# Optimization experiments

Measured on AMD Instinct MI355X. Metric: run time of the kernel, lower is better.

## Reference

```python
import jax, jax.numpy as jnp
import numpy as np

B, S, D_IN, D_OUT, HID, E, SHARE, TOPK = 4, 2048, 1024, 1024, 2048, 8, 1, 2


def setup_inputs() -> dict:
    key = jax.random.key(0)
    ks = jax.random.split(key, 12)
    s_in = 1.0 / np.sqrt(D_IN)
    s_hid = 1.0 / np.sqrt(HID)
    return {
        "x": jax.random.normal(ks[0], (B, S, D_IN), jnp.float32),
        "gate_w": jax.random.normal(ks[1], (D_IN, E), jnp.float32) * s_in,
        "gate_b": jnp.zeros((E,), jnp.float32),
        "ew1": jax.random.normal(ks[2], (E, D_IN, HID), jnp.float32) * s_in,
        "eb1": jnp.zeros((E, HID), jnp.float32),
        "ew2": jax.random.normal(ks[3], (E, HID, D_OUT), jnp.float32) * s_hid,
        "eb2": jnp.zeros((E, D_OUT), jnp.float32),
        "sw1": jax.random.normal(ks[4], (SHARE, D_IN, HID), jnp.float32) * s_in,
        "sb1": jnp.zeros((SHARE, HID), jnp.float32),
        "sw2": jax.random.normal(ks[5], (SHARE, HID, D_OUT), jnp.float32) * s_hid,
        "sb2": jnp.zeros((SHARE, D_OUT), jnp.float32),
        "top_k": TOPK,
    }


def reference(x, gate_w, gate_b, ew1, eb1, ew2, eb2, sw1, sb1, sw2, sb2, top_k):
    Bx, Sx, Din = x.shape
    flat_x = x.reshape(-1, Din)                      # [T, D]
    T = flat_x.shape[0]
    Ex = gate_w.shape[1]

    # gate + softmax + top-k, renormalize top-k weights
    logits = flat_x @ gate_w + gate_b                # [T, E]
    expert_weights = jax.nn.softmax(logits, axis=-1)
    topv, topi = jax.lax.top_k(expert_weights, top_k)
    topv = topv / jnp.sum(topv, axis=-1, keepdims=True)

    # per-token combine weights scattered into [T, E] (zero for unselected)
    combine = jnp.zeros((T, Ex), flat_x.dtype)
    combine = combine.at[jnp.arange(T)[:, None], topi].add(topv)

    # expert MLPs (BasicExpert: Linear -> ReLU -> Linear), batched over experts
    h = jax.nn.relu(jnp.einsum("td,edh->teh", flat_x, ew1) + eb1)   # [T, E, H]
    eo = jnp.einsum("teh,eho->teo", h, ew2) + eb2                    # [T, E, O]
    moe_out = jnp.einsum("teo,te->to", eo, combine)                  # [T, O]
    final = moe_out.reshape(Bx, Sx, -1)

    # shared experts added densely to every token
    for k in range(sw1.shape[0]):
        sh = jax.nn.relu(jnp.einsum("bsd,dh->bsh", x, sw1[k]) + sb1[k])
        final = final + jnp.einsum("bsh,ho->bso", sh, sw2[k]) + sb2[k]

    return final, expert_weights
```

## Files before the change

### kernel.cpp

```cpp
#include <hip/hip_runtime.h>
#include <hip/hip_bf16.h>
#include <stdint.h>

#define T_TOK 8192
#define DIN   1024
#define DOUT  1024
#define HID   2048
#define NEXP  8
#define MAXN  8192

typedef __attribute__((ext_vector_type(8))) short short8;
typedef __attribute__((ext_vector_type(4))) float floatx4;

__device__ __forceinline__ ushort f2bf(float f) {
    uint32_t u = __float_as_uint(f);
    uint32_t r = (u + 0x7fffu + ((u >> 16) & 1u)) >> 16;
    return (ushort)r;
}

__global__ void convert_x_kernel(const float* __restrict__ in, ushort* __restrict__ out, int n4) {
    int i = blockIdx.x * blockDim.x + threadIdx.x;
    if (i >= n4) return;
    float4 v = ((const float4*)in)[i];
    ushort4 o;
    o.x = f2bf(v.x); o.y = f2bf(v.y); o.z = f2bf(v.z); o.w = f2bf(v.w);
    ((ushort4*)out)[i] = o;
}

__global__ void transpose_bf16_kernel(const float* __restrict__ in, ushort* __restrict__ out,
                                      int R, int C) {
    __shared__ float tile[64][65];
    size_t base = (size_t)blockIdx.z * R * C;
    in  += base;
    out += base;
    int r0 = blockIdx.y * 64, c0 = blockIdx.x * 64;
    int t  = threadIdx.x;
    int rr = t >> 4;
    int cc = (t & 15) * 4;
    for (int p = 0; p < 4; p++) {
        int row = rr + p * 16;
        float4 v = *(const float4*)(in + (size_t)(r0 + row) * C + c0 + cc);
        tile[row][cc + 0] = v.x; tile[row][cc + 1] = v.y;
        tile[row][cc + 2] = v.z; tile[row][cc + 3] = v.w;
    }
    __syncthreads();
    for (int p = 0; p < 4; p++) {
        int orow = rr + p * 16;
        ushort4 o;
        o.x = f2bf(tile[cc + 0][orow]);
        o.y = f2bf(tile[cc + 1][orow]);
        o.z = f2bf(tile[cc + 2][orow]);
        o.w = f2bf(tile[cc + 3][orow]);
        *(ushort4*)(out + (size_t)(c0 + orow) * R + r0 + cc) = o;
    }
}

__global__ void gate_kernel(const float* __restrict__ x, const float* __restrict__ gw,
                            const float* __restrict__ gb, float* __restrict__ ew_out,
                            int* __restrict__ counts, int* __restrict__ expert_tok,
                            float* __restrict__ expert_w) {
    int gid  = blockIdx.x * blockDim.x + threadIdx.x;
    int t    = gid >> 6;
    int lane = threadIdx.x & 63;
    if (t >= T_TOK) return;
    float acc[8];
    #pragma unroll
    for (int e = 0; e < 8; e++) acc[e] = 0.f;
    const float* xrow = x + (size_t)t * DIN;
    #pragma unroll
    for (int i = 0; i < 16; i++) {
        int d = lane + i * 64;
        float xv = xrow[d];
        const float4* wr = (const float4*)(gw + (size_t)d * 8);
        float4 w0 = wr[0], w1 = wr[1];
        acc[0] += xv * w0.x; acc[1] += xv * w0.y; acc[2] += xv * w0.z; acc[3] += xv * w0.w;
        acc[4] += xv * w1.x; acc[5] += xv * w1.y; acc[6] += xv * w1.z; acc[7] += xv * w1.w;
    }
    #pragma unroll
    for (int e = 0; e < 8; e++)
        #pragma unroll
        for (int off = 32; off; off >>= 1) acc[e] += __shfl_xor(acc[e], off);
    if (lane == 0) {
        float l[8], mx = -1e30f;
        #pragma unroll
        for (int e = 0; e < 8; e++) { l[e] = acc[e] + gb[e]; mx = fmaxf(mx, l[e]); }
        float s = 0.f;
        #pragma unroll
        for (int e = 0; e < 8; e++) { l[e] = expf(l[e] - mx); s += l[e]; }
        float inv = 1.f / s;
        #pragma unroll
        for (int e = 0; e < 8; e++) { l[e] *= inv; ew_out[(size_t)t * 8 + e] = l[e]; }
        int i1 = 0;
        #pragma unroll
        for (int e = 1; e < 8; e++) if (l[e] > l[i1]) i1 = e;
        int i2 = (i1 == 0) ? 1 : 0;
        #pragma unroll
        for (int e = 0; e < 8; e++) if (e != i1 && l[e] > l[i2]) i2 = e;
        float s2 = l[i1] + l[i2];
        float w1v = l[i1] / s2, w2v = l[i2] / s2;
        int r1 = atomicAdd(&counts[i1], 1);
        expert_tok[i1 * MAXN + r1] = t;
        expert_w [i1 * MAXN + r1] = w1v;
        int r2 = atomicAdd(&counts[i2], 1);
        expert_tok[i2 * MAXN + r2] = t;
        expert_w [i2 * MAXN + r2] = w2v;
    }
}

__global__ void prefix_kernel(const int* __restrict__ counts, int* __restrict__ offsets) {
    if (threadIdx.x == 0 && blockIdx.x == 0) {
        int o = 0;
        for (int e = 0; e < NEXP; e++) { offsets[e] = o; o += counts[e]; }
    }
}

template <int MODE>
__global__ __launch_bounds__(256)
void gemm_kernel(const ushort* __restrict__ A, const ushort* __restrict__ Bt,
                 const float* __restrict__ bias, ushort* __restrict__ Hout,
                 float* __restrict__ Out,
                 const int* __restrict__ counts, const int* __restrict__ offsets,
                 const int* __restrict__ expert_tok, const float* __restrict__ expert_w,
                 int K) {
    const int e = blockIdx.z;
    int cnt, rowbase = 0;
    size_t bt_off = 0;
    const float* bcol = bias;
    if constexpr (MODE == 0) {
        cnt = counts[e]; rowbase = offsets[e];
        bt_off = (size_t)e * HID * DIN; bcol = bias + (size_t)e * HID;
    } else if constexpr (MODE == 1) {
        cnt = T_TOK;
    } else if constexpr (MODE == 2) {
        cnt = counts[e]; rowbase = offsets[e];
        bt_off = (size_t)e * DOUT * HID; bcol = bias + (size_t)e * DOUT;
    } else {
        cnt = T_TOK;
    }

    const int m0 = blockIdx.y * 128;
    if (m0 >= cnt) return;
    const int n0 = blockIdx.x * 128;

    __shared__ ushort As[128][72];
    __shared__ ushort Bs[128][72];
    __shared__ int    rowA[128];
    __shared__ int    rowTok[128];
    __shared__ float  rowW[128];

    const int tid = threadIdx.x;
    if (tid < 128) {
        int g = m0 + tid;
        if constexpr (MODE == 0) {
            rowA[tid] = (g < cnt) ? expert_tok[e * MAXN + g] : 0;
        } else if constexpr (MODE == 1) {
            rowA[tid] = g;
        } else if constexpr (MODE == 2) {
            rowA[tid]   = (g < cnt) ? (rowbase + g) : rowbase;
            rowTok[tid] = (g < cnt) ? expert_tok[e * MAXN + g] : 0;
            rowW[tid]   = (g < cnt) ? expert_w[e * MAXN + g] : 0.f;
        } else {
            rowA[tid] = g;
        }
    }
    __syncthreads();

    floatx4 acc[4][4];
    #pragma unroll
    for (int i = 0; i < 4; i++)
        #pragma unroll
        for (int j = 0; j < 4; j++) acc[i][j] = (floatx4){0.f, 0.f, 0.f, 0.f};

    const int wave = tid >> 6, lane = tid & 63;
    const int wm = (wave >> 1) * 64, wn = (wave & 1) * 64;
    const int lm = lane & 15, lq = lane >> 4;
    const int arow_s = tid >> 3;
    const int achunk = (tid & 7) * 8;

    for (int k0 = 0; k0 < K; k0 += 64) {
        #pragma unroll
        for (int i = 0; i < 4; i++) {
            int r = arow_s + i * 32;
            const ushort* srca = A + (size_t)rowA[r] * K + k0 + achunk;
            *(uint4*)(&As[r][achunk]) = *(const uint4*)srca;
            const ushort* srcb = Bt + bt_off + (size_t)(n0 + r) * K + k0 + achunk;
            *(uint4*)(&Bs[r][achunk]) = *(const uint4*)srcb;
        }
        __syncthreads();
        #pragma unroll
        for (int kk = 0; kk < 64; kk += 32) {
            short8 afr[4], bfr[4];
            #pragma unroll
            for (int mt = 0; mt < 4; mt++)
                afr[mt] = *(const short8*)(&As[wm + mt * 16 + lm][kk + lq * 8]);
            #pragma unroll
            for (int nt = 0; nt < 4; nt++)
                bfr[nt] = *(const short8*)(&Bs[wn + nt * 16 + lm][kk + lq * 8]);
            #pragma unroll
            for (int mt = 0; mt < 4; mt++)
                #pragma unroll
                for (int nt = 0; nt < 4; nt++)
                    acc[mt][nt] = __builtin_amdgcn_mfma_f32_16x16x32_bf16(
                        afr[mt], bfr[nt], acc[mt][nt], 0, 0, 0);
        }
        __syncthreads();
    }

    #pragma unroll
    for (int mt = 0; mt < 4; mt++) {
        int rl_base = wm + mt * 16 + lq * 4;
        #pragma unroll
        for (int nt = 0; nt < 4; nt++) {
            int col = n0 + wn + nt * 16 + lm;
            float bv = bcol[col];
            #pragma unroll
            for (int r = 0; r < 4; r++) {
                int rl = rl_base + r;
                int g  = m0 + rl;
                float v = acc[mt][nt][r];
                if constexpr (MODE == 0) {
                    if (g < cnt) {
                        v = fmaxf(v + bv, 0.f);
                        Hout[(size_t)(rowbase + g) * HID + col] = f2bf(v);
                    }
                } else if constexpr (MODE == 1) {
                    v = fmaxf(v + bv, 0.f);
                    Hout[(size_t)g * HID + col] = f2bf(v);
                } else if constexpr (MODE == 2) {
                    if (g < cnt) {
                        v = (v + bv) * rowW[rl];
                        atomicAdd(&Out[(size_t)rowTok[rl] * DOUT + col], v);
                    }
                } else {
                    atomicAdd(&Out[(size_t)g * DOUT + col], v + bv);
                }
            }
        }
    }
}

extern "C" void kernel_launch(void* const* d_in, const int* in_sizes, int n_in,
                              void* d_out, int out_size, void* d_ws, size_t ws_size,
                              hipStream_t stream) {
    const float* x   = (const float*)d_in[0];
    const float* gw  = (const float*)d_in[1];
    const float* gb  = (const float*)d_in[2];
    const float* ew1 = (const float*)d_in[3];
    const float* eb1 = (const float*)d_in[4];
    const float* ew2 = (const float*)d_in[5];
    const float* eb2 = (const float*)d_in[6];
    const float* sw1 = (const float*)d_in[7];
    const float* sb1 = (const float*)d_in[8];
    const float* sw2 = (const float*)d_in[9];
    const float* sb2 = (const float*)d_in[10];

    float* out_final = (float*)d_out;
    float* out_ew    = out_final + (size_t)T_TOK * DOUT;

    char* ws = (char*)d_ws;
    size_t off = 0;
    auto alloc = [&](size_t bytes) -> void* {
        void* p = ws + off;
        off += (bytes + 255) & ~(size_t)255;
        return p;
    };
    ushort* x_bf    = (ushort*)alloc((size_t)T_TOK * DIN * 2);
    ushort* ew1t    = (ushort*)alloc((size_t)NEXP * HID * DIN * 2);
    ushort* ew2t    = (ushort*)alloc((size_t)NEXP * DOUT * HID * 2);
    ushort* sw1t    = (ushort*)alloc((size_t)HID * DIN * 2);
    ushort* sw2t    = (ushort*)alloc((size_t)DOUT * HID * 2);
    ushort* h_buf   = (ushort*)alloc((size_t)T_TOK * 2 * HID * 2);
    ushort* sh_buf  = (ushort*)alloc((size_t)T_TOK * HID * 2);
    int*    counts  = (int*)alloc(NEXP * 4);
    int*    offsets = (int*)alloc(NEXP * 4);
    int*    etok    = (int*)alloc((size_t)NEXP * MAXN * 4);
    float*  ew      = (float*)alloc((size_t)NEXP * MAXN * 4);

    hipMemsetAsync(d_out, 0, (size_t)T_TOK * DOUT * 4, stream);
    hipMemsetAsync(counts, 0, NEXP * 4, stream);

    convert_x_kernel<<<(T_TOK * DIN / 4) / 256, 256, 0, stream>>>(x, x_bf, T_TOK * DIN / 4);
    transpose_bf16_kernel<<<dim3(HID / 64, DIN / 64, NEXP), 256, 0, stream>>>(ew1, ew1t, DIN, HID);
    transpose_bf16_kernel<<<dim3(DOUT / 64, HID / 64, NEXP), 256, 0, stream>>>(ew2, ew2t, HID, DOUT);
    transpose_bf16_kernel<<<dim3(HID / 64, DIN / 64, 1), 256, 0, stream>>>(sw1, sw1t, DIN, HID);
    transpose_bf16_kernel<<<dim3(DOUT / 64, HID / 64, 1), 256, 0, stream>>>(sw2, sw2t, HID, DOUT);

    gate_kernel<<<T_TOK / 4, 256, 0, stream>>>(x, gw, gb, out_ew, counts, etok, ew);
    prefix_kernel<<<1, 64, 0, stream>>>(counts, offsets);

    gemm_kernel<0><<<dim3(HID / 128, MAXN / 128, NEXP), 256, 0, stream>>>(
        x_bf, ew1t, eb1, h_buf, nullptr, counts, offsets, etok, ew, DIN);
    gemm_kernel<1><<<dim3(HID / 128, T_TOK / 128, 1), 256, 0, stream>>>(
        x_bf, sw1t, sb1, sh_buf, nullptr, counts, offsets, etok, ew, DIN);
    gemm_kernel<2><<<dim3(DOUT / 128, MAXN / 128, NEXP), 256, 0, stream>>>(
        h_buf, ew2t, eb2, nullptr, out_final, counts, offsets, etok, ew, HID);
    gemm_kernel<3><<<dim3(DOUT / 128, T_TOK / 128, 1), 256, 0, stream>>>(
        sh_buf, sw2t, sb2, nullptr, out_final, counts, offsets, etok, ew, HID);
}
```

Baseline: 810.9 us.

## Load GEMM tiles directly to LDS and build expert lists with block-local atomics

The GEMM mainloop now uses global_load_lds to copy 16-byte chunks straight into shared memory, skipping the register round trip. The LDS tile is stored in an MFMA-fragment-ordered layout so each lane reads a contiguous short8. Gating is split into a per-token compute kernel and a list-building kernel that first counts in shared memory, then does one global atomic per expert per block. This removes the contention of per-token global atomics, at the cost of an extra launch and some scratch buffers. The direct-to-LDS path still loads and waits on one buffer, so there is no overlap between loading and compute.

```diff
diff --git a/kernel.cpp b/kernel.cpp
--- a/kernel.cpp
+++ b/kernel.cpp
@@ -16,6 +16,12 @@
     uint32_t u = __float_as_uint(f);
     uint32_t r = (u + 0x7fffu + ((u >> 16) & 1u)) >> 16;
     return (ushort)r;
+}
+
+__device__ __forceinline__ void load_lds_16(const ushort* g, ushort* l) {
+    __builtin_amdgcn_global_load_lds(
+        (const __attribute__((address_space(1))) void*)g,
+        (__attribute__((address_space(3))) void*)l, 16, 0, 0);
 }
 
 __global__ void convert_x_kernel(const float* __restrict__ in, ushort* __restrict__ out, int n4) {
@@ -55,10 +61,10 @@
     }
 }
 
-__global__ void gate_kernel(const float* __restrict__ x, const float* __restrict__ gw,
-                            const float* __restrict__ gb, float* __restrict__ ew_out,
-                            int* __restrict__ counts, int* __restrict__ expert_tok,
-                            float* __restrict__ expert_w) {
+__global__ void gate_compute_kernel(const float* __restrict__ x, const float* __restrict__ gw,
+                                    const float* __restrict__ gb, float* __restrict__ ew_out,
+                                    int* __restrict__ te1, int* __restrict__ te2,
+                                    float* __restrict__ tw1, float* __restrict__ tw2) {
     int gid  = blockIdx.x * blockDim.x + threadIdx.x;
     int t    = gid >> 6;
     int lane = threadIdx.x & 63;
@@ -97,14 +103,34 @@
         #pragma unroll
         for (int e = 0; e < 8; e++) if (e != i1 && l[e] > l[i2]) i2 = e;
         float s2 = l[i1] + l[i2];
-        float w1v = l[i1] / s2, w2v = l[i2] / s2;
-        int r1 = atomicAdd(&counts[i1], 1);
-        expert_tok[i1 * MAXN + r1] = t;
-        expert_w [i1 * MAXN + r1] = w1v;
-        int r2 = atomicAdd(&counts[i2], 1);
-        expert_tok[i2 * MAXN + r2] = t;
-        expert_w [i2 * MAXN + r2] = w2v;
-    }
+        te1[t] = i1; tw1[t] = l[i1] / s2;
+        te2[t] = i2; tw2[t] = l[i2] / s2;
+    }
+}
+
+__global__ void build_lists_kernel(const int* __restrict__ te1, const int* __restrict__ te2,
+                                   const float* __restrict__ tw1, const float* __restrict__ tw2,
+                                   int* __restrict__ counts, int* __restrict__ etok,
+                                   float* __restrict__ ew) {
+    __shared__ int lcnt[NEXP];
+    __shared__ int gbase[NEXP];
+    int tid = threadIdx.x;
+    int t = blockIdx.x * 256 + tid;
+    if (tid < NEXP) lcnt[tid] = 0;
+    __syncthreads();
+    int e1 = te1[t], e2 = te2[t];
+    float w1 = tw1[t], w2 = tw2[t];
+    int r1 = atomicAdd(&lcnt[e1], 1);
+    int r2 = atomicAdd(&lcnt[e2], 1);
+    __syncthreads();
+    if (tid < NEXP) gbase[tid] = atomicAdd(&counts[tid], lcnt[tid]);
+    __syncthreads();
+    int s1 = gbase[e1] + r1;
+    etok[e1 * MAXN + s1] = t;
+    ew  [e1 * MAXN + s1] = w1;
+    int s2 = gbase[e2] + r2;
+    etok[e2 * MAXN + s2] = t;
+    ew  [e2 * MAXN + s2] = w2;
 }
 
 __global__ void prefix_kernel(const int* __restrict__ counts, int* __restrict__ offsets) {
@@ -142,8 +168,8 @@
     if (m0 >= cnt) return;
     const int n0 = blockIdx.x * 128;
 
-    __shared__ ushort As[128][72];
-    __shared__ ushort Bs[128][72];
+    __shared__ ushort As[8192];
+    __shared__ ushort Bs[8192];
     __shared__ int    rowA[128];
     __shared__ int    rowTok[128];
     __shared__ float  rowW[128];
@@ -165,37 +191,46 @@
     }
     __syncthreads();
 
+    const int wave = tid >> 6, lane = tid & 63;
+    const int lm = lane & 15, lq = lane >> 4;
+
+    const ushort* gA[4];
+    const ushort* gB[4];
+    ushort* dA[4];
+    ushort* dB[4];
+    #pragma unroll
+    for (int i = 0; i < 4; i++) {
+        int b = wave * 4 + i;
+        int rblk = b >> 1, kkb = b & 1;
+        int r = rblk * 16 + lm;
+        gA[i] = A + (size_t)rowA[r] * K + kkb * 32 + lq * 8;
+        gB[i] = Bt + bt_off + (size_t)(n0 + r) * K + kkb * 32 + lq * 8;
+        dA[i] = &As[b * 512];
+        dB[i] = &Bs[b * 512];
+    }
+
     floatx4 acc[4][4];
     #pragma unroll
     for (int i = 0; i < 4; i++)
         #pragma unroll
         for (int j = 0; j < 4; j++) acc[i][j] = (floatx4){0.f, 0.f, 0.f, 0.f};
 
-    const int wave = tid >> 6, lane = tid & 63;
-    const int wm = (wave >> 1) * 64, wn = (wave & 1) * 64;
-    const int lm = lane & 15, lq = lane >> 4;
-    const int arow_s = tid >> 3;
-    const int achunk = (tid & 7) * 8;
-
     for (int k0 = 0; k0 < K; k0 += 64) {
         #pragma unroll
         for (int i = 0; i < 4; i++) {
-            int r = arow_s + i * 32;
-            const ushort* srca = A + (size_t)rowA[r] * K + k0 + achunk;
-            *(uint4*)(&As[r][achunk]) = *(const uint4*)srca;
-            const ushort* srcb = Bt + bt_off + (size_t)(n0 + r) * K + k0 + achunk;
-            *(uint4*)(&Bs[r][achunk]) = *(const uint4*)srcb;
+            load_lds_16(gA[i] + k0, dA[i]);
+            load_lds_16(gB[i] + k0, dB[i]);
         }
         __syncthreads();
         #pragma unroll
-        for (int kk = 0; kk < 64; kk += 32) {
+        for (int kkb = 0; kkb < 2; kkb++) {
             short8 afr[4], bfr[4];
             #pragma unroll
             for (int mt = 0; mt < 4; mt++)
-                afr[mt] = *(const short8*)(&As[wm + mt * 16 + lm][kk + lq * 8]);
+                afr[mt] = *(const short8*)&As[(((wave >> 1) * 4 + mt) * 2 + kkb) * 512 + lane * 8];
             #pragma unroll
             for (int nt = 0; nt < 4; nt++)
-                bfr[nt] = *(const short8*)(&Bs[wn + nt * 16 + lm][kk + lq * 8]);
+                bfr[nt] = *(const short8*)&Bs[(((wave & 1) * 4 + nt) * 2 + kkb) * 512 + lane * 8];
             #pragma unroll
             for (int mt = 0; mt < 4; mt++)
                 #pragma unroll
@@ -206,6 +241,7 @@
         __syncthreads();
     }
 
+    const int wm = (wave >> 1) * 64, wn = (wave & 1) * 64;
     #pragma unroll
     for (int mt = 0; mt < 4; mt++) {
         int rl_base = wm + mt * 16 + lq * 4;
@@ -275,6 +311,10 @@
     int*    offsets = (int*)alloc(NEXP * 4);
     int*    etok    = (int*)alloc((size_t)NEXP * MAXN * 4);
     float*  ew      = (float*)alloc((size_t)NEXP * MAXN * 4);
+    int*    te1     = (int*)alloc((size_t)T_TOK * 4);
+    int*    te2     = (int*)alloc((size_t)T_TOK * 4);
+    float*  tw1     = (float*)alloc((size_t)T_TOK * 4);
+    float*  tw2     = (float*)alloc((size_t)T_TOK * 4);
 
     hipMemsetAsync(d_out, 0, (size_t)T_TOK * DOUT * 4, stream);
     hipMemsetAsync(counts, 0, NEXP * 4, stream);
@@ -285,7 +325,8 @@
     transpose_bf16_kernel<<<dim3(HID / 64, DIN / 64, 1), 256, 0, stream>>>(sw1, sw1t, DIN, HID);
     transpose_bf16_kernel<<<dim3(DOUT / 64, HID / 64, 1), 256, 0, stream>>>(sw2, sw2t, HID, DOUT);
 
-    gate_kernel<<<T_TOK / 4, 256, 0, stream>>>(x, gw, gb, out_ew, counts, etok, ew);
+    gate_compute_kernel<<<T_TOK / 4, 256, 0, stream>>>(x, gw, gb, out_ew, te1, te2, tw1, tw2);
+    build_lists_kernel<<<T_TOK / 256, 256, 0, stream>>>(te1, te2, tw1, tw2, counts, etok, ew);
     prefix_kernel<<<1, 64, 0, stream>>>(counts, offsets);
 
     gemm_kernel<0><<<dim3(HID / 128, MAXN / 128, NEXP), 256, 0, stream>>>(
```

Result: no change. 800.0 us (-1.4%).
